# Optimization experiments

Measured on AMD Instinct MI355X. Metric: run time of the kernel, lower is better.

The kernel has to match this reference:

```python
import jax, jax.numpy as jnp
import numpy as np

DIM_SOL = 4096
DIM_CONTEXT = 4096
DIM_HIDDEN = 8192
INIT = 0.01  # matches nn.Parameter uniform_(-0.01, 0.01)


def setup_inputs() -> dict:
    key = jax.random.key(0)
    k1, k2, k3, k4, k5, k6 = jax.random.split(key, 6)
    context = jax.random.normal(k1, (DIM_CONTEXT,), dtype=jnp.float32)
    # per-step uniforms driving the Bernoulli samples
    u = jax.random.uniform(k2, (DIM_SOL,), dtype=jnp.float32)
    W = jax.random.uniform(k3, (DIM_HIDDEN, DIM_CONTEXT + DIM_SOL), dtype=jnp.float32, minval=-INIT, maxval=INIT)
    V = jax.random.uniform(k4, (DIM_SOL, DIM_HIDDEN), dtype=jnp.float32, minval=-INIT, maxval=INIT)
    b = jax.random.uniform(k5, (DIM_SOL,), dtype=jnp.float32, minval=-INIT, maxval=INIT)
    c = jax.random.uniform(k6, (DIM_HIDDEN,), dtype=jnp.float32, minval=-INIT, maxval=INIT)
    return {"context": context, "u": u, "W": W, "V": V, "b": b, "c": c}


def reference(context, u, W, V, b, c):
    dim_sol = V.shape[0]
    dim_context = context.shape[0]
    dtype = context.dtype

    # a_0 = c + W[:, :dim_context] @ context
    a0 = c + W[:, :dim_context] @ context  # (dim_hidden,)
    W_sol = W[:, dim_context:].T           # (dim_sol, dim_hidden), column i per step

    # Torch returns log(p_val[dim_sol-2]) = sum of the first (dim_sol-2) log-factors.
    mask = (jnp.arange(dim_sol) < dim_sol - 2).astype(dtype)

    def step(carry, xs):
        a, logp = carry
        ui, Vi, bi, Wi, mi = xs
        h = jax.nn.sigmoid(a)                          # (dim_hidden,)
        p = jax.nn.sigmoid(bi + Vi @ h)                # scalar: P(x_i = 1 | x_<i, c)
        s = jax.lax.stop_gradient((ui < p).astype(dtype))  # detached Bernoulli sample
        # log( p^s * (1-p)^(1-s) ), accumulated in log space
        logp = logp + mi * (s * jnp.log(p) + (1.0 - s) * jnp.log1p(-p))
        a = a + Wi * s
        return (a, logp), s

    (_, logp), sol = jax.lax.scan(step, (a0, jnp.zeros((), dtype)), (u, V, b, W_sol, mask))
    return sol[:, None], logp  # solution shape (dim_sol, 1) matches T.stack of (1,) samples
```

## Files before the change

kernel.cpp:

```cpp
#include <hip/hip_runtime.h>
#include <cstdint>
#include <cstddef>

#define DIM_SOL 4096
#define DIM_CTX 4096
#define DIM_HID 8192
#define NWG 32
#define NROUND (DIM_SOL / 4)


__device__ __forceinline__ float sigmoid_precise(float x) {
    return 1.0f / (1.0f + expf(-x));
}
__device__ __forceinline__ float hsig(float x) {
    return __builtin_amdgcn_rcpf(1.0f + __expf(-x));
}

__global__ __launch_bounds__(256) void ar_prep(
    const float* __restrict__ W, const float* __restrict__ context,
    const float* __restrict__ c, float* __restrict__ a0,
    float* __restrict__ Wp, int packed)
{
    const int wg  = blockIdx.x;
    const int tid = threadIdx.x;

    if (wg < 256) {
        const int wave = wg * 4 + (tid >> 6);
        const int lane = tid & 63;
        const float4* ctx4 = reinterpret_cast<const float4*>(context);
        const int r0 = wave * 8;
        for (int r = r0; r < r0 + 8; ++r) {
            const float4* Wr4 = reinterpret_cast<const float4*>(W + (size_t)r * DIM_HID);
            float acc = 0.f;
#pragma unroll
            for (int j = 0; j < 16; ++j) {
                float4 w4 = Wr4[lane + 64 * j];
                float4 x4 = ctx4[lane + 64 * j];
                acc = fmaf(w4.x, x4.x, acc);
                acc = fmaf(w4.y, x4.y, acc);
                acc = fmaf(w4.z, x4.z, acc);
                acc = fmaf(w4.w, x4.w, acc);
            }
#pragma unroll
            for (int off = 32; off >= 1; off >>= 1) acc += __shfl_xor(acc, off);
            if (lane == 0) a0[r] = c[r] + acc;
        }
    } else if (packed) {
        __shared__ float tile[64][65];
        const int tx = tid & 63, ty = tid >> 6;
        for (int t = wg - 256; t < 64 * 128; t += 1792) {
            const int i0 = (t & 63) * 64;
            const int k0 = (t >> 6) * 64;
            __syncthreads();
#pragma unroll
            for (int dy = 0; dy < 64; dy += 4) {
                tile[dy + ty][tx] =
                    W[(size_t)(k0 + dy + ty) * DIM_HID + (DIM_CTX + i0 + tx)];
            }
            __syncthreads();
#pragma unroll
            for (int dy = 0; dy < 64; dy += 4) {
                Wp[(size_t)(i0 + dy + ty) * DIM_HID + (k0 + tx)] = tile[tx][dy + ty];
            }
        }
    }
}

__global__ __launch_bounds__(256) void ar_serial(
    const float* __restrict__ V, const float* __restrict__ W,
    const float* __restrict__ b, const float* __restrict__ u,
    const float* __restrict__ a0, const float* __restrict__ Wp,
    unsigned long long* __restrict__ pub,
    float* __restrict__ pbuf, float* __restrict__ out, int packed)
{
    const int g   = blockIdx.x;
    const int tid = threadIdx.x;
    const int wv  = tid >> 6;
    const int l   = tid & 63;
    const int w   = l & 15;
    const int sb  = l >> 4;
    const int e   = g * 256 + tid;

    __shared__ float lred[2][64];

    const float4* b4 = reinterpret_cast<const float4*>(b);
    const float4* u4 = reinterpret_cast<const float4*>(u);

    float a = a0[e];

    auto loadW = [&](int i) -> float {
        if (packed) return Wp[(size_t)i * DIM_HID + e];
        return W[(size_t)e * DIM_HID + DIM_CTX + i];
    };

    float Vr0 = V[(size_t)0 * DIM_HID + e], Vr1 = V[(size_t)1 * DIM_HID + e];
    float Vr2 = V[(size_t)2 * DIM_HID + e], Vr3 = V[(size_t)3 * DIM_HID + e];
    float Wr0 = loadW(0), Wr1 = loadW(1), Wr2 = loadW(2), Wr3 = loadW(3);
    float4 bb = b4[0], uu = u4[0];

    for (int r = 0; r < NROUND; ++r) {
        const unsigned tag = (unsigned)(r + 1);
        unsigned long long* bank = pub + (size_t)(r & 1) * 512;

        const float x1 = a + Wr0;
        const float x2 = a + Wr1;
        const float x3 = x1 + Wr1;
        const float x4 = a + Wr2;
        const float x5 = x1 + Wr2;
        const float x6 = x2 + Wr2;
        const float x7 = x3 + Wr2;
        const float h0 = hsig(a),  h1 = hsig(x1), h2 = hsig(x2), h3 = hsig(x3);
        const float h4 = hsig(x4), h5 = hsig(x5), h6 = hsig(x6), h7 = hsig(x7);

        float S[16];
        S[0] = Vr0 * h0;
        S[1] = Vr1 * h0;  S[2] = Vr1 * h1;
        S[3] = Vr2 * h0;  S[4] = Vr2 * h1;  S[5] = Vr2 * h2;  S[6] = Vr2 * h3;
        S[7] = Vr3 * h0;  S[8] = Vr3 * h1;  S[9] = Vr3 * h2;  S[10] = Vr3 * h3;
        S[11] = Vr3 * h4; S[12] = Vr3 * h5; S[13] = Vr3 * h6; S[14] = Vr3 * h7;
        S[15] = 0.0f;

        {
            const bool hi1 = l & 1;
            float o[8];
#pragma unroll
            for (int j = 0; j < 8; ++j) {
                o[j] = hi1 ? S[2 * j] : S[2 * j + 1];
                S[j] = hi1 ? S[2 * j + 1] : S[2 * j];
            }
#pragma unroll
            for (int j = 0; j < 8; ++j) S[j] += __shfl_xor(o[j], 1);
        }
        {
            const bool hi2 = l & 2;
            float o[4];
#pragma unroll
            for (int j = 0; j < 4; ++j) {
                o[j] = hi2 ? S[2 * j] : S[2 * j + 1];
                S[j] = hi2 ? S[2 * j + 1] : S[2 * j];
            }
#pragma unroll
            for (int j = 0; j < 4; ++j) S[j] += __shfl_xor(o[j], 2);
        }
        {
            const bool hi3 = l & 4;
            float o[2];
#pragma unroll
            for (int j = 0; j < 2; ++j) {
                o[j] = hi3 ? S[2 * j] : S[2 * j + 1];
                S[j] = hi3 ? S[2 * j + 1] : S[2 * j];
            }
#pragma unroll
            for (int j = 0; j < 2; ++j) S[j] += __shfl_xor(o[j], 4);
        }
        {
            const bool hi4 = l & 8;
            float o0 = hi4 ? S[0] : S[1];
            float k0 = hi4 ? S[1] : S[0];
            S[0] = k0 + __shfl_xor(o0, 8);
        }
        float T = S[0];
        T += __shfl_xor(T, 16);
        T += __shfl_xor(T, 32);

        if (l < 16) lred[r & 1][w * 4 + wv] = T;
        __syncthreads();
        if (wv == 0 && l < 15) {
            const float4 q = *reinterpret_cast<const float4*>(&lred[r & 1][w * 4]);
            const float Twg = ((q.x + q.y) + q.z) + q.w;
            unsigned long long v =
                ((unsigned long long)__float_as_uint(Twg) << 32) |
                (unsigned long long)tag;
            __hip_atomic_store(bank + (size_t)g * 16 + w, v,
                               __ATOMIC_RELAXED, __HIP_MEMORY_SCOPE_AGENT);
        }

        float Vn0, Vn1, Vn2, Vn3, Wn0, Wn1, Wn2, Wn3;
        float4 bbn, uun;
        if (r + 1 < NROUND) {
            const int i1 = 4 * (r + 1);
            Vn0 = V[(size_t)(i1 + 0) * DIM_HID + e];
            Vn1 = V[(size_t)(i1 + 1) * DIM_HID + e];
            Vn2 = V[(size_t)(i1 + 2) * DIM_HID + e];
            Vn3 = V[(size_t)(i1 + 3) * DIM_HID + e];
            Wn0 = loadW(i1 + 0); Wn1 = loadW(i1 + 1);
            Wn2 = loadW(i1 + 2); Wn3 = loadW(i1 + 3);
            bbn = b4[r + 1]; uun = u4[r + 1];
        }

        unsigned long long q0, q1, q2, q3, q4, q5, q6, q7;
        {
            unsigned long long* ms = bank + (size_t)sb * 16 + w;
            bool ok = (w == 15);
            for (;;) {
                if (!ok) {
                    q0 = __hip_atomic_load(ms + 0 * 64, __ATOMIC_RELAXED, __HIP_MEMORY_SCOPE_AGENT);
                    q1 = __hip_atomic_load(ms + 1 * 64, __ATOMIC_RELAXED, __HIP_MEMORY_SCOPE_AGENT);
                    q2 = __hip_atomic_load(ms + 2 * 64, __ATOMIC_RELAXED, __HIP_MEMORY_SCOPE_AGENT);
                    q3 = __hip_atomic_load(ms + 3 * 64, __ATOMIC_RELAXED, __HIP_MEMORY_SCOPE_AGENT);
                    q4 = __hip_atomic_load(ms + 4 * 64, __ATOMIC_RELAXED, __HIP_MEMORY_SCOPE_AGENT);
                    q5 = __hip_atomic_load(ms + 5 * 64, __ATOMIC_RELAXED, __HIP_MEMORY_SCOPE_AGENT);
                    q6 = __hip_atomic_load(ms + 6 * 64, __ATOMIC_RELAXED, __HIP_MEMORY_SCOPE_AGENT);
                    q7 = __hip_atomic_load(ms + 7 * 64, __ATOMIC_RELAXED, __HIP_MEMORY_SCOPE_AGENT);
                    ok = ((unsigned)q0 == tag) & ((unsigned)q1 == tag) &
                         ((unsigned)q2 == tag) & ((unsigned)q3 == tag) &
                         ((unsigned)q4 == tag) & ((unsigned)q5 == tag) &
                         ((unsigned)q6 == tag) & ((unsigned)q7 == tag);
                }
                if (__all(ok)) break;
            }
        }
        float G;
        {
            float p0 = __uint_as_float((unsigned)(q0 >> 32));
            float p1 = __uint_as_float((unsigned)(q1 >> 32));
            float p2 = __uint_as_float((unsigned)(q2 >> 32));
            float p3 = __uint_as_float((unsigned)(q3 >> 32));
            float p4 = __uint_as_float((unsigned)(q4 >> 32));
            float p5 = __uint_as_float((unsigned)(q5 >> 32));
            float p6 = __uint_as_float((unsigned)(q6 >> 32));
            float p7 = __uint_as_float((unsigned)(q7 >> 32));
            G = (w == 15) ? 0.0f
                          : ((((((p0 + p1) + p2) + p3) + p4) + p5) + p6) + p7;
        }
        G += __shfl_xor(G, 16);
        G += __shfl_xor(G, 32);

        const float T0 = __shfl(G, 0),  T1 = __shfl(G, 1),  T2 = __shfl(G, 2);
        const float T3 = __shfl(G, 3),  T4 = __shfl(G, 4),  T5 = __shfl(G, 5);
        const float T6 = __shfl(G, 6),  T7 = __shfl(G, 7),  T8 = __shfl(G, 8);
        const float T9 = __shfl(G, 9),  T10 = __shfl(G, 10), T11 = __shfl(G, 11);
        const float T12 = __shfl(G, 12), T13 = __shfl(G, 13), T14 = __shfl(G, 14);

        const float p0 = sigmoid_precise(bb.x + T0);
        const bool  s0 = uu.x < p0;
        const float p1 = sigmoid_precise(bb.y + (s0 ? T2 : T1));
        const bool  s1 = uu.y < p1;
        const float t2a = s0 ? T4 : T3, t2b = s0 ? T6 : T5;
        const float p2 = sigmoid_precise(bb.z + (s1 ? t2b : t2a));
        const bool  s2 = uu.z < p2;
        const float t3a = s0 ? T8 : T7,   t3b = s0 ? T10 : T9;
        const float t3c = s0 ? T12 : T11, t3d = s0 ? T14 : T13;
        const float t3e = s1 ? t3b : t3a, t3f = s1 ? t3d : t3c;
        const float p3 = sigmoid_precise(bb.w + (s2 ? t3f : t3e));
        const bool  s3 = uu.w < p3;

        if (g == 0 && tid == 0) {
            const int i = 4 * r;
            float4 so; so.x = s0 ? 1.f : 0.f; so.y = s1 ? 1.f : 0.f;
            so.z = s2 ? 1.f : 0.f; so.w = s3 ? 1.f : 0.f;
            *reinterpret_cast<float4*>(out + i) = so;
            float4 po; po.x = p0; po.y = p1; po.z = p2; po.w = p3;
            *reinterpret_cast<float4*>(pbuf + i) = po;
        }

        if (s0) a += Wr0;
        if (s1) a += Wr1;
        if (s2) a += Wr2;
        if (s3) a += Wr3;

        Vr0 = Vn0; Vr1 = Vn1; Vr2 = Vn2; Vr3 = Vn3;
        Wr0 = Wn0; Wr1 = Wn1; Wr2 = Wn2; Wr3 = Wn3;
        bb = bbn; uu = uun;
    }
}

__global__ __launch_bounds__(256) void ar_logp(
    const float* __restrict__ pbuf, float* __restrict__ out)
{
    __shared__ float red[256];
    const int t = threadIdx.x;
    float acc = 0.f;
    for (int i = t; i < DIM_SOL - 2; i += 256) {
        const float p = pbuf[i];
        const float s = out[i];
        acc += (s > 0.5f) ? logf(p) : log1pf(-p);
    }
    red[t] = acc;
    __syncthreads();
    for (int wdt = 128; wdt >= 1; wdt >>= 1) {
        if (t < wdt) red[t] += red[t + wdt];
        __syncthreads();
    }
    if (t == 0) out[DIM_SOL] = red[0];
}

extern "C" void kernel_launch(void* const* d_in, const int* in_sizes, int n_in,
                              void* d_out, int out_size, void* d_ws, size_t ws_size,
                              hipStream_t stream)
{
    const float* context = (const float*)d_in[0];
    const float* u       = (const float*)d_in[1];
    const float* W       = (const float*)d_in[2];
    const float* V       = (const float*)d_in[3];
    const float* b       = (const float*)d_in[4];
    const float* c       = (const float*)d_in[5];
    float* out = (float*)d_out;

    char* ws = (char*)d_ws;
    unsigned long long* pub = (unsigned long long*)(ws);
    float* pbuf = (float*)(ws + 8192);
    float* a0   = (float*)(ws + 24576);
    float* Wp   = (float*)(ws + 65536);
    const size_t wp_bytes = (size_t)DIM_SOL * DIM_HID * sizeof(float);
    const int packed = (ws_size >= (size_t)65536 + wp_bytes) ? 1 : 0;

    hipLaunchKernelGGL(ar_prep, dim3(2048), dim3(256), 0, stream,
                       W, context, c, a0, Wp, packed);
    hipLaunchKernelGGL(ar_serial, dim3(NWG), dim3(256), 0, stream,
                       V, W, b, u, a0, Wp, pub, pbuf, out, packed);
    hipLaunchKernelGGL(ar_logp, dim3(1), dim3(256), 0, stream, pbuf, out);
}
```

Before: 2.757 ms.

## Speculate six sampling steps per grid-wide sync round instead of four

Each round now evaluates every hidden-state hypothesis for the next six Bernoulli samples (32 sigmoid branches and 63 partial dot products) instead of four. That cuts the number of cross-workgroup publish/poll synchronisation rounds from 1024 to 683. The reduction is widened to a full 64-lane butterfly, the published mailbox holds 64 words per workgroup, and a shared-memory table feeds the serial sample-selection tree. In exchange, each round does more sigmoid evaluation, shuffling and an extra __syncthreads, and the workspace now deliberately places pbuf on top of a0.

```diff
diff --git a/kernel.cpp b/kernel.cpp
--- a/kernel.cpp
+++ b/kernel.cpp
@@ -6,7 +6,8 @@
 #define DIM_CTX 4096
 #define DIM_HID 8192
 #define NWG 32
-#define NROUND (DIM_SOL / 4)
+#define KSTEP 6
+#define NROUND ((DIM_SOL + KSTEP - 1) / KSTEP)
 
 
 __device__ __forceinline__ float sigmoid_precise(float x) {
@@ -66,25 +67,21 @@
     }
 }
 
-__global__ __launch_bounds__(256) void ar_serial(
+__global__ __launch_bounds__(256, 1) void ar_serial(
     const float* __restrict__ V, const float* __restrict__ W,
     const float* __restrict__ b, const float* __restrict__ u,
-    const float* __restrict__ a0, const float* __restrict__ Wp,
+    const float* a0, const float* __restrict__ Wp,
     unsigned long long* __restrict__ pub,
-    float* __restrict__ pbuf, float* __restrict__ out, int packed)
+    float* pbuf, float* __restrict__ out, int packed)
 {
     const int g   = blockIdx.x;
     const int tid = threadIdx.x;
     const int wv  = tid >> 6;
     const int l   = tid & 63;
-    const int w   = l & 15;
-    const int sb  = l >> 4;
     const int e   = g * 256 + tid;
 
-    __shared__ float lred[2][64];
-
-    const float4* b4 = reinterpret_cast<const float4*>(b);
-    const float4* u4 = reinterpret_cast<const float4*>(u);
+    __shared__ float lred[2][4][64];
+    __shared__ float tot[64];
 
     float a = a0[e];
 
@@ -93,115 +90,133 @@
         return W[(size_t)e * DIM_HID + DIM_CTX + i];
     };
 
-    float Vr0 = V[(size_t)0 * DIM_HID + e], Vr1 = V[(size_t)1 * DIM_HID + e];
-    float Vr2 = V[(size_t)2 * DIM_HID + e], Vr3 = V[(size_t)3 * DIM_HID + e];
-    float Wr0 = loadW(0), Wr1 = loadW(1), Wr2 = loadW(2), Wr3 = loadW(3);
-    float4 bb = b4[0], uu = u4[0];
+    float Vr[KSTEP], Wr[KSTEP], bc[KSTEP], uc[KSTEP];
+#pragma unroll
+    for (int j = 0; j < KSTEP; ++j) {
+        Vr[j] = V[(size_t)j * DIM_HID + e];
+        Wr[j] = loadW(j);
+        bc[j] = b[j];
+        uc[j] = u[j];
+    }
 
     for (int r = 0; r < NROUND; ++r) {
         const unsigned tag = (unsigned)(r + 1);
-        unsigned long long* bank = pub + (size_t)(r & 1) * 512;
-
-        const float x1 = a + Wr0;
-        const float x2 = a + Wr1;
-        const float x3 = x1 + Wr1;
-        const float x4 = a + Wr2;
-        const float x5 = x1 + Wr2;
-        const float x6 = x2 + Wr2;
-        const float x7 = x3 + Wr2;
-        const float h0 = hsig(a),  h1 = hsig(x1), h2 = hsig(x2), h3 = hsig(x3);
-        const float h4 = hsig(x4), h5 = hsig(x5), h6 = hsig(x6), h7 = hsig(x7);
-
-        float S[16];
-        S[0] = Vr0 * h0;
-        S[1] = Vr1 * h0;  S[2] = Vr1 * h1;
-        S[3] = Vr2 * h0;  S[4] = Vr2 * h1;  S[5] = Vr2 * h2;  S[6] = Vr2 * h3;
-        S[7] = Vr3 * h0;  S[8] = Vr3 * h1;  S[9] = Vr3 * h2;  S[10] = Vr3 * h3;
-        S[11] = Vr3 * h4; S[12] = Vr3 * h5; S[13] = Vr3 * h6; S[14] = Vr3 * h7;
-        S[15] = 0.0f;
-
-        {
-            const bool hi1 = l & 1;
-            float o[8];
-#pragma unroll
-            for (int j = 0; j < 8; ++j) {
-                o[j] = hi1 ? S[2 * j] : S[2 * j + 1];
-                S[j] = hi1 ? S[2 * j + 1] : S[2 * j];
-            }
-#pragma unroll
-            for (int j = 0; j < 8; ++j) S[j] += __shfl_xor(o[j], 1);
-        }
-        {
-            const bool hi2 = l & 2;
-            float o[4];
-#pragma unroll
-            for (int j = 0; j < 4; ++j) {
-                o[j] = hi2 ? S[2 * j] : S[2 * j + 1];
-                S[j] = hi2 ? S[2 * j + 1] : S[2 * j];
-            }
-#pragma unroll
-            for (int j = 0; j < 4; ++j) S[j] += __shfl_xor(o[j], 2);
-        }
-        {
-            const bool hi3 = l & 4;
-            float o[2];
-#pragma unroll
-            for (int j = 0; j < 2; ++j) {
-                o[j] = hi3 ? S[2 * j] : S[2 * j + 1];
-                S[j] = hi3 ? S[2 * j + 1] : S[2 * j];
-            }
-#pragma unroll
-            for (int j = 0; j < 2; ++j) S[j] += __shfl_xor(o[j], 4);
-        }
-        {
-            const bool hi4 = l & 8;
-            float o0 = hi4 ? S[0] : S[1];
-            float k0 = hi4 ? S[1] : S[0];
-            S[0] = k0 + __shfl_xor(o0, 8);
-        }
-        float T = S[0];
-        T += __shfl_xor(T, 16);
-        T += __shfl_xor(T, 32);
-
-        if (l < 16) lred[r & 1][w * 4 + wv] = T;
+        unsigned long long* bank = pub + (size_t)(r & 1) * (32 * 64);
+
+        float xs[32];
+        xs[0] = a;
+        xs[1] = xs[0] + Wr[0];
+        xs[2] = xs[0] + Wr[1];
+        xs[3] = xs[1] + Wr[1];
+#pragma unroll
+        for (int m = 0; m < 4; ++m)  xs[4 + m]  = xs[m] + Wr[2];
+#pragma unroll
+        for (int m = 0; m < 8; ++m)  xs[8 + m]  = xs[m] + Wr[3];
+#pragma unroll
+        for (int m = 0; m < 16; ++m) xs[16 + m] = xs[m] + Wr[4];
+
+        float h[32];
+#pragma unroll
+        for (int m = 0; m < 32; ++m) h[m] = hsig(xs[m]);
+
+        float S[64];
+        S[0] = Vr[0] * h[0];
+#pragma unroll
+        for (int m = 0; m < 2; ++m)  S[1 + m]  = Vr[1] * h[m];
+#pragma unroll
+        for (int m = 0; m < 4; ++m)  S[3 + m]  = Vr[2] * h[m];
+#pragma unroll
+        for (int m = 0; m < 8; ++m)  S[7 + m]  = Vr[3] * h[m];
+#pragma unroll
+        for (int m = 0; m < 16; ++m) S[15 + m] = Vr[4] * h[m];
+#pragma unroll
+        for (int m = 0; m < 32; ++m) S[31 + m] = Vr[5] * h[m];
+        S[63] = 0.0f;
+
+        {
+            const bool hi = l & 1; float o[32];
+#pragma unroll
+            for (int j = 0; j < 32; ++j) { o[j] = hi ? S[2*j] : S[2*j+1]; S[j] = hi ? S[2*j+1] : S[2*j]; }
+#pragma unroll
+            for (int j = 0; j < 32; ++j) S[j] += __shfl_xor(o[j], 1);
+        }
+        {
+            const bool hi = l & 2; float o[16];
+#pragma unroll
+            for (int j = 0; j < 16; ++j) { o[j] = hi ? S[2*j] : S[2*j+1]; S[j] = hi ? S[2*j+1] : S[2*j]; }
+#pragma unroll
+            for (int j = 0; j < 16; ++j) S[j] += __shfl_xor(o[j], 2);
+        }
+        {
+            const bool hi = l & 4; float o[8];
+#pragma unroll
+            for (int j = 0; j < 8; ++j) { o[j] = hi ? S[2*j] : S[2*j+1]; S[j] = hi ? S[2*j+1] : S[2*j]; }
+#pragma unroll
+            for (int j = 0; j < 8; ++j) S[j] += __shfl_xor(o[j], 4);
+        }
+        {
+            const bool hi = l & 8; float o[4];
+#pragma unroll
+            for (int j = 0; j < 4; ++j) { o[j] = hi ? S[2*j] : S[2*j+1]; S[j] = hi ? S[2*j+1] : S[2*j]; }
+#pragma unroll
+            for (int j = 0; j < 4; ++j) S[j] += __shfl_xor(o[j], 8);
+        }
+        {
+            const bool hi = l & 16; float o[2];
+#pragma unroll
+            for (int j = 0; j < 2; ++j) { o[j] = hi ? S[2*j] : S[2*j+1]; S[j] = hi ? S[2*j+1] : S[2*j]; }
+#pragma unroll
+            for (int j = 0; j < 2; ++j) S[j] += __shfl_xor(o[j], 16);
+        }
+        {
+            const bool hi = l & 32;
+            float o = hi ? S[0] : S[1];
+            float k = hi ? S[1] : S[0];
+            S[0] = k + __shfl_xor(o, 32);
+        }
+
+        lred[r & 1][wv][l] = S[0];
         __syncthreads();
-        if (wv == 0 && l < 15) {
-            const float4 q = *reinterpret_cast<const float4*>(&lred[r & 1][w * 4]);
-            const float Twg = ((q.x + q.y) + q.z) + q.w;
+        if (wv == 0 && l < 63) {
+            const float Twg = ((lred[r & 1][0][l] + lred[r & 1][1][l]) +
+                                lred[r & 1][2][l]) + lred[r & 1][3][l];
             unsigned long long v =
                 ((unsigned long long)__float_as_uint(Twg) << 32) |
                 (unsigned long long)tag;
-            __hip_atomic_store(bank + (size_t)g * 16 + w, v,
+            __hip_atomic_store(bank + (size_t)g * 64 + l, v,
                                __ATOMIC_RELAXED, __HIP_MEMORY_SCOPE_AGENT);
         }
 
-        float Vn0, Vn1, Vn2, Vn3, Wn0, Wn1, Wn2, Wn3;
-        float4 bbn, uun;
+        float Vn[KSTEP], Wn[KSTEP], bn[KSTEP], un[KSTEP];
         if (r + 1 < NROUND) {
-            const int i1 = 4 * (r + 1);
-            Vn0 = V[(size_t)(i1 + 0) * DIM_HID + e];
-            Vn1 = V[(size_t)(i1 + 1) * DIM_HID + e];
-            Vn2 = V[(size_t)(i1 + 2) * DIM_HID + e];
-            Vn3 = V[(size_t)(i1 + 3) * DIM_HID + e];
-            Wn0 = loadW(i1 + 0); Wn1 = loadW(i1 + 1);
-            Wn2 = loadW(i1 + 2); Wn3 = loadW(i1 + 3);
-            bbn = b4[r + 1]; uun = u4[r + 1];
-        }
-
-        unsigned long long q0, q1, q2, q3, q4, q5, q6, q7;
-        {
-            unsigned long long* ms = bank + (size_t)sb * 16 + w;
-            bool ok = (w == 15);
+            const int i1 = KSTEP * (r + 1);
+#pragma unroll
+            for (int j = 0; j < KSTEP; ++j) {
+                int idx = i1 + j;
+                if (idx > DIM_SOL - 1) idx = DIM_SOL - 1;
+                Vn[j] = V[(size_t)idx * DIM_HID + e];
+                Wn[j] = loadW(idx);
+                bn[j] = b[idx];
+                un[j] = u[idx];
+            }
+        }
+
+        const int word = wv * 16 + (l & 15);
+        {
+            unsigned long long q0 = 0, q1 = 0, q2 = 0, q3 = 0,
+                               q4 = 0, q5 = 0, q6 = 0, q7 = 0;
+            unsigned long long* ms = bank + (size_t)(l >> 4) * 64 + word;
+            bool ok = (word == 63);
             for (;;) {
                 if (!ok) {
-                    q0 = __hip_atomic_load(ms + 0 * 64, __ATOMIC_RELAXED, __HIP_MEMORY_SCOPE_AGENT);
-                    q1 = __hip_atomic_load(ms + 1 * 64, __ATOMIC_RELAXED, __HIP_MEMORY_SCOPE_AGENT);
-                    q2 = __hip_atomic_load(ms + 2 * 64, __ATOMIC_RELAXED, __HIP_MEMORY_SCOPE_AGENT);
-                    q3 = __hip_atomic_load(ms + 3 * 64, __ATOMIC_RELAXED, __HIP_MEMORY_SCOPE_AGENT);
-                    q4 = __hip_atomic_load(ms + 4 * 64, __ATOMIC_RELAXED, __HIP_MEMORY_SCOPE_AGENT);
-                    q5 = __hip_atomic_load(ms + 5 * 64, __ATOMIC_RELAXED, __HIP_MEMORY_SCOPE_AGENT);
-                    q6 = __hip_atomic_load(ms + 6 * 64, __ATOMIC_RELAXED, __HIP_MEMORY_SCOPE_AGENT);
-                    q7 = __hip_atomic_load(ms + 7 * 64, __ATOMIC_RELAXED, __HIP_MEMORY_SCOPE_AGENT);
+                    q0 = __hip_atomic_load(ms + 0 * 256, __ATOMIC_RELAXED, __HIP_MEMORY_SCOPE_AGENT);
+                    q1 = __hip_atomic_load(ms + 1 * 256, __ATOMIC_RELAXED, __HIP_MEMORY_SCOPE_AGENT);
+                    q2 = __hip_atomic_load(ms + 2 * 256, __ATOMIC_RELAXED, __HIP_MEMORY_SCOPE_AGENT);
+                    q3 = __hip_atomic_load(ms + 3 * 256, __ATOMIC_RELAXED, __HIP_MEMORY_SCOPE_AGENT);
+                    q4 = __hip_atomic_load(ms + 4 * 256, __ATOMIC_RELAXED, __HIP_MEMORY_SCOPE_AGENT);
+                    q5 = __hip_atomic_load(ms + 5 * 256, __ATOMIC_RELAXED, __HIP_MEMORY_SCOPE_AGENT);
+                    q6 = __hip_atomic_load(ms + 6 * 256, __ATOMIC_RELAXED, __HIP_MEMORY_SCOPE_AGENT);
+                    q7 = __hip_atomic_load(ms + 7 * 256, __ATOMIC_RELAXED, __HIP_MEMORY_SCOPE_AGENT);
                     ok = ((unsigned)q0 == tag) & ((unsigned)q1 == tag) &
                          ((unsigned)q2 == tag) & ((unsigned)q3 == tag) &
                          ((unsigned)q4 == tag) & ((unsigned)q5 == tag) &
@@ -209,59 +224,99 @@
                 }
                 if (__all(ok)) break;
             }
-        }
-        float G;
-        {
-            float p0 = __uint_as_float((unsigned)(q0 >> 32));
-            float p1 = __uint_as_float((unsigned)(q1 >> 32));
-            float p2 = __uint_as_float((unsigned)(q2 >> 32));
-            float p3 = __uint_as_float((unsigned)(q3 >> 32));
-            float p4 = __uint_as_float((unsigned)(q4 >> 32));
-            float p5 = __uint_as_float((unsigned)(q5 >> 32));
-            float p6 = __uint_as_float((unsigned)(q6 >> 32));
-            float p7 = __uint_as_float((unsigned)(q7 >> 32));
-            G = (w == 15) ? 0.0f
-                          : ((((((p0 + p1) + p2) + p3) + p4) + p5) + p6) + p7;
-        }
-        G += __shfl_xor(G, 16);
-        G += __shfl_xor(G, 32);
-
-        const float T0 = __shfl(G, 0),  T1 = __shfl(G, 1),  T2 = __shfl(G, 2);
-        const float T3 = __shfl(G, 3),  T4 = __shfl(G, 4),  T5 = __shfl(G, 5);
-        const float T6 = __shfl(G, 6),  T7 = __shfl(G, 7),  T8 = __shfl(G, 8);
-        const float T9 = __shfl(G, 9),  T10 = __shfl(G, 10), T11 = __shfl(G, 11);
-        const float T12 = __shfl(G, 12), T13 = __shfl(G, 13), T14 = __shfl(G, 14);
-
-        const float p0 = sigmoid_precise(bb.x + T0);
-        const bool  s0 = uu.x < p0;
-        const float p1 = sigmoid_precise(bb.y + (s0 ? T2 : T1));
-        const bool  s1 = uu.y < p1;
-        const float t2a = s0 ? T4 : T3, t2b = s0 ? T6 : T5;
-        const float p2 = sigmoid_precise(bb.z + (s1 ? t2b : t2a));
-        const bool  s2 = uu.z < p2;
-        const float t3a = s0 ? T8 : T7,   t3b = s0 ? T10 : T9;
-        const float t3c = s0 ? T12 : T11, t3d = s0 ? T14 : T13;
-        const float t3e = s1 ? t3b : t3a, t3f = s1 ? t3d : t3c;
-        const float p3 = sigmoid_precise(bb.w + (s2 ? t3f : t3e));
-        const bool  s3 = uu.w < p3;
+            float G;
+            {
+                float p0 = __uint_as_float((unsigned)(q0 >> 32));
+                float p1 = __uint_as_float((unsigned)(q1 >> 32));
+                float p2 = __uint_as_float((unsigned)(q2 >> 32));
+                float p3 = __uint_as_float((unsigned)(q3 >> 32));
+                float p4 = __uint_as_float((unsigned)(q4 >> 32));
+                float p5 = __uint_as_float((unsigned)(q5 >> 32));
+                float p6 = __uint_as_float((unsigned)(q6 >> 32));
+                float p7 = __uint_as_float((unsigned)(q7 >> 32));
+                G = (word == 63) ? 0.0f
+                                 : ((((((p0 + p1) + p2) + p3) + p4) + p5) + p6) + p7;
+            }
+            G += __shfl_xor(G, 16);
+            G += __shfl_xor(G, 32);
+            if (l < 16) tot[word] = G;
+        }
+        __syncthreads();
+
+        float t1[2], t2[4], t3[8], t4[16], t5[32];
+        const float T0 = tot[0];
+#pragma unroll
+        for (int j = 0; j < 2; ++j)  t1[j] = tot[1 + j];
+#pragma unroll
+        for (int j = 0; j < 4; ++j)  t2[j] = tot[3 + j];
+#pragma unroll
+        for (int j = 0; j < 8; ++j)  t3[j] = tot[7 + j];
+#pragma unroll
+        for (int j = 0; j < 16; ++j) t4[j] = tot[15 + j];
+#pragma unroll
+        for (int j = 0; j < 32; ++j) t5[j] = tot[31 + j];
+
+        const float p0 = sigmoid_precise(bc[0] + T0);
+        const bool  s0 = uc[0] < p0;
+
+        const float p1 = sigmoid_precise(bc[1] + (s0 ? t1[1] : t1[0]));
+        const bool  s1 = uc[1] < p1;
+
+#pragma unroll
+        for (int j = 0; j < 2; ++j)  t2[j] = s0 ? t2[2*j+1] : t2[2*j];
+        const float p2 = sigmoid_precise(bc[2] + (s1 ? t2[1] : t2[0]));
+        const bool  s2 = uc[2] < p2;
+
+#pragma unroll
+        for (int j = 0; j < 4; ++j)  t3[j] = s0 ? t3[2*j+1] : t3[2*j];
+#pragma unroll
+        for (int j = 0; j < 2; ++j)  t3[j] = s1 ? t3[2*j+1] : t3[2*j];
+        const float p3 = sigmoid_precise(bc[3] + (s2 ? t3[1] : t3[0]));
+        const bool  s3 = uc[3] < p3;
+
+#pragma unroll
+        for (int j = 0; j < 8; ++j)  t4[j] = s0 ? t4[2*j+1] : t4[2*j];
+#pragma unroll
+        for (int j = 0; j < 4; ++j)  t4[j] = s1 ? t4[2*j+1] : t4[2*j];
+#pragma unroll
+        for (int j = 0; j < 2; ++j)  t4[j] = s2 ? t4[2*j+1] : t4[2*j];
+        const float p4 = sigmoid_precise(bc[4] + (s3 ? t4[1] : t4[0]));
+        const bool  s4 = uc[4] < p4;
+
+#pragma unroll
+        for (int j = 0; j < 16; ++j) t5[j] = s0 ? t5[2*j+1] : t5[2*j];
+#pragma unroll
+        for (int j = 0; j < 8; ++j)  t5[j] = s1 ? t5[2*j+1] : t5[2*j];
+#pragma unroll
+        for (int j = 0; j < 4; ++j)  t5[j] = s2 ? t5[2*j+1] : t5[2*j];
+#pragma unroll
+        for (int j = 0; j < 2; ++j)  t5[j] = s3 ? t5[2*j+1] : t5[2*j];
+        const float p5 = sigmoid_precise(bc[5] + (s4 ? t5[1] : t5[0]));
+        const bool  s5 = uc[5] < p5;
 
         if (g == 0 && tid == 0) {
-            const int i = 4 * r;
-            float4 so; so.x = s0 ? 1.f : 0.f; so.y = s1 ? 1.f : 0.f;
-            so.z = s2 ? 1.f : 0.f; so.w = s3 ? 1.f : 0.f;
-            *reinterpret_cast<float4*>(out + i) = so;
-            float4 po; po.x = p0; po.y = p1; po.z = p2; po.w = p3;
-            *reinterpret_cast<float4*>(pbuf + i) = po;
-        }
-
-        if (s0) a += Wr0;
-        if (s1) a += Wr1;
-        if (s2) a += Wr2;
-        if (s3) a += Wr3;
-
-        Vr0 = Vn0; Vr1 = Vn1; Vr2 = Vn2; Vr3 = Vn3;
-        Wr0 = Wn0; Wr1 = Wn1; Wr2 = Wn2; Wr3 = Wn3;
-        bb = bbn; uu = uun;
+            const int i0 = KSTEP * r;
+            out[i0 + 0] = s0 ? 1.f : 0.f;  pbuf[i0 + 0] = p0;
+            out[i0 + 1] = s1 ? 1.f : 0.f;  pbuf[i0 + 1] = p1;
+            out[i0 + 2] = s2 ? 1.f : 0.f;  pbuf[i0 + 2] = p2;
+            out[i0 + 3] = s3 ? 1.f : 0.f;  pbuf[i0 + 3] = p3;
+            if (i0 + 4 < DIM_SOL) { out[i0 + 4] = s4 ? 1.f : 0.f; pbuf[i0 + 4] = p4; }
+            if (i0 + 5 < DIM_SOL) { out[i0 + 5] = s5 ? 1.f : 0.f; pbuf[i0 + 5] = p5; }
+        }
+
+        if (s0) a += Wr[0];
+        if (s1) a += Wr[1];
+        if (s2) a += Wr[2];
+        if (s3) a += Wr[3];
+        if (s4) a += Wr[4];
+        if (s5) a += Wr[5];
+
+        if (r + 1 < NROUND) {
+#pragma unroll
+            for (int j = 0; j < KSTEP; ++j) {
+                Vr[j] = Vn[j]; Wr[j] = Wn[j]; bc[j] = bn[j]; uc[j] = un[j];
+            }
+        }
     }
 }
 
@@ -299,8 +354,8 @@
 
     char* ws = (char*)d_ws;
     unsigned long long* pub = (unsigned long long*)(ws);
-    float* pbuf = (float*)(ws + 8192);
-    float* a0   = (float*)(ws + 24576);
+    float* a0   = (float*)(ws + 32768);
+    float* pbuf = (float*)(ws + 32768);
     float* Wp   = (float*)(ws + 65536);
     const size_t wp_bytes = (size_t)DIM_SOL * DIM_HID * sizeof(float);
     const int packed = (ws_size >= (size_t)65536 + wp_bytes) ? 1 : 0;
```

Measured after the change: 2.818 ms. 2.2% more time.
